# Optimization experiments

Hardware: AMD Instinct MI355X
Metric: run time of the kernel (lower is better)

The kernel has to match this reference:

```python
import jax, jax.numpy as jnp
import numpy as np

EMBED = 256
HEADS = 8
LAYERS = 6
FFN = 1024
LEVELS = 4
POINTS = 4
SHAPES = [(128, 128), (64, 64), (32, 32), (16, 16)]


def setup_inputs() -> dict:
    key = jax.random.key(0)
    ks = jax.random.split(key, 32)
    B = 2
    inp = {}
    for i, (h, w) in enumerate(SHAPES):
        inp[f'src{i}'] = jax.random.normal(ks[i], (B, EMBED, h, w), jnp.float32)
        inp[f'pos{i}'] = jax.random.normal(ks[4 + i], (B, EMBED, h, w), jnp.float32)
    s = 0.02
    inp['level_embed'] = jax.random.normal(ks[8], (LEVELS, EMBED), jnp.float32) * s
    inp['Wv'] = jax.random.normal(ks[9], (LAYERS, EMBED, EMBED), jnp.float32) * s
    inp['bv'] = jnp.zeros((LAYERS, EMBED), jnp.float32)
    inp['Woff'] = jax.random.normal(ks[10], (LAYERS, EMBED, HEADS * LEVELS * POINTS * 2), jnp.float32) * s
    inp['boff'] = jax.random.normal(ks[11], (LAYERS, HEADS * LEVELS * POINTS * 2), jnp.float32) * 0.5
    inp['Waw'] = jax.random.normal(ks[12], (LAYERS, EMBED, HEADS * LEVELS * POINTS), jnp.float32) * s
    inp['baw'] = jnp.zeros((LAYERS, HEADS * LEVELS * POINTS), jnp.float32)
    inp['Wout'] = jax.random.normal(ks[13], (LAYERS, EMBED, EMBED), jnp.float32) * s
    inp['bout'] = jnp.zeros((LAYERS, EMBED), jnp.float32)
    inp['gamma'] = jnp.ones((LAYERS, EMBED), jnp.float32)
    inp['beta'] = jnp.zeros((LAYERS, EMBED), jnp.float32)
    inp['W1'] = jax.random.normal(ks[14], (LAYERS, EMBED, FFN), jnp.float32) * s
    inp['b1'] = jnp.zeros((LAYERS, FFN), jnp.float32)
    inp['W2'] = jax.random.normal(ks[15], (LAYERS, FFN, EMBED), jnp.float32) * s
    inp['b2'] = jnp.zeros((LAYERS, EMBED), jnp.float32)
    return inp


def _layernorm(x, g, b, eps=1e-5):
    mu = x.mean(-1, keepdims=True)
    var = ((x - mu) ** 2).mean(-1, keepdims=True)
    return (x - mu) * jax.lax.rsqrt(var + eps) * g + b


def _bilinear_sample(value, loc, Hl, Wl):
    # value: [B, heads, S_l, Dh]; loc: [B, Len, heads, P, 2] normalized to [0,1]
    # grid_sample semantics: align_corners=False, zero padding
    B, Len, heads, P, _ = loc.shape
    Dh = value.shape[-1]
    x = loc[..., 0] * Wl - 0.5
    y = loc[..., 1] * Hl - 0.5
    x0 = jnp.floor(x)
    y0 = jnp.floor(y)
    dx = x - x0
    dy = y - y0
    x0i = x0.astype(jnp.int32)
    y0i = y0.astype(jnp.int32)
    out = jnp.zeros((B, heads, Len, P, Dh), value.dtype)
    corners = [(x0i, y0i, (1 - dx) * (1 - dy)), (x0i + 1, y0i, dx * (1 - dy)),
               (x0i, y0i + 1, (1 - dx) * dy), (x0i + 1, y0i + 1, dx * dy)]
    for xi, yi, w in corners:
        valid = (xi >= 0) & (xi < Wl) & (yi >= 0) & (yi < Hl)
        idx = jnp.clip(yi, 0, Hl - 1) * Wl + jnp.clip(xi, 0, Wl - 1)  # [B,Len,heads,P]
        idx_t = idx.transpose(0, 2, 1, 3).reshape(B, heads, Len * P)
        g = jnp.take_along_axis(value, idx_t[..., None], axis=2)  # [B,heads,Len*P,Dh]
        g = g.reshape(B, heads, Len, P, Dh)
        wv = jnp.where(valid, w, 0.0).transpose(0, 2, 1, 3)[..., None]  # [B,heads,Len,P,1]
        out = out + g * wv
    return out


def reference(src0, src1, src2, src3, pos0, pos1, pos2, pos3, level_embed,
              Wv, bv, Woff, boff, Waw, baw, Wout, bout, gamma, beta, W1, b1, W2, b2):
    srcs = [src0, src1, src2, src3]
    poss = [pos0, pos1, pos2, pos3]
    B, C = src0.shape[0], src0.shape[1]
    shapes = [(s.shape[2], s.shape[3]) for s in srcs]
    L = len(shapes)
    heads, P = HEADS, POINTS
    Dh = C // heads
    x = jnp.concatenate([s.reshape(B, C, -1).transpose(0, 2, 1) for s in srcs], axis=1)  # [B,Len,C]
    pos_flat = jnp.concatenate(
        [p.reshape(B, C, -1).transpose(0, 2, 1) + level_embed[l][None, None, :]
         for l, p in enumerate(poss)], axis=1)
    starts = np.concatenate([[0], np.cumsum([h * w for h, w in shapes])[:-1]]).tolist()
    # reference points (valid_ratios are all ones since masks are all-False)
    refs = []
    for (H, W) in shapes:
        yy, xx = jnp.meshgrid(jnp.linspace(0.5, H - 0.5, H), jnp.linspace(0.5, W - 0.5, W), indexing='ij')
        refs.append(jnp.stack([xx.reshape(-1) / W, yy.reshape(-1) / H], axis=-1))
    ref = jnp.concatenate(refs, axis=0)  # [Len,2]
    normalizer = jnp.array([[w, h] for h, w in shapes], dtype=x.dtype)  # [L,2]
    Len = x.shape[1]
    for li in range(LAYERS):
        q = x + pos_flat
        off = (q @ Woff[li] + boff[li]).reshape(B, Len, heads, L, P, 2)
        aw = jax.nn.softmax((q @ Waw[li] + baw[li]).reshape(B, Len, heads, L * P), axis=-1)
        aw = aw.reshape(B, Len, heads, L, P)
        loc = ref[None, :, None, None, None, :] + off / normalizer[None, None, None, :, None, :]
        v = (x @ Wv[li] + bv[li]).reshape(B, Len, heads, Dh).transpose(0, 2, 1, 3)  # [B,heads,Len,Dh]
        acc = jnp.zeros((B, heads, Len, Dh), x.dtype)
        for lvl, (H, W) in enumerate(shapes):
            s0 = starts[lvl]
            vl = v[:, :, s0:s0 + H * W, :]
            samp = _bilinear_sample(vl, loc[:, :, :, lvl], H, W)  # [B,heads,Len,P,Dh]
            awl = aw[:, :, :, lvl].transpose(0, 2, 1, 3)  # [B,heads,Len,P]
            acc = acc + (samp * awl[..., None]).sum(axis=3)
        attn_out = acc.transpose(0, 2, 1, 3).reshape(B, Len, C) @ Wout[li] + bout[li]
        x = x + attn_out  # dropout is identity at eval
        x = _layernorm(x, gamma[li], beta[li])
        x = jax.nn.relu(x @ W1[li] + b1[li]) @ W2[li] + b2[li]  # Mlp output (no residual, per source)
    return x
```

## Files before the change

kernel.cpp:

```cpp
#include <hip/hip_runtime.h>

#define LEN 21760
#define MROWS 43520
#define WSTRIDE 753664

typedef __attribute__((ext_vector_type(8))) short s8v;
typedef __attribute__((ext_vector_type(4))) short s4v;
typedef __attribute__((ext_vector_type(4))) float f4v;
typedef __attribute__((ext_vector_type(4))) unsigned u4v;

__device__ inline float bf2f(short u){
  union { unsigned u; float f; } v; v.u = ((unsigned)(unsigned short)u) << 16; return v.f;
}
__device__ inline short f2bf(float f){
  union { float f; unsigned u; } v; v.f = f;
  unsigned r = v.u + 0x7fffu + ((v.u >> 16) & 1u);
  return (short)(r >> 16);
}
__device__ inline void gload_lds16(const short* g, short* l){
  __builtin_amdgcn_global_load_lds((const __attribute__((address_space(1))) void*)g,
                                   (__attribute__((address_space(3))) void*)l, 16, 0, 0);
}

__global__ __launch_bounds__(256) void prep_kernel(
    const float* __restrict__ s0,const float* __restrict__ s1,
    const float* __restrict__ s2,const float* __restrict__ s3,
    const float* __restrict__ p0,const float* __restrict__ p1,
    const float* __restrict__ p2,const float* __restrict__ p3,
    const float* __restrict__ le,
    short* __restrict__ xbf, short* __restrict__ posb,
    short* __restrict__ q)
{
  __shared__ float xs[64][65];
  __shared__ float ps[64][65];
  const int n0 = blockIdx.x * 64;
  const int b  = blockIdx.y;
  const int t  = threadIdx.x;

  int l, s0n, lw;
  if (n0 < 16384){ l=0; s0n=0; lw=7; }
  else if (n0 < 20480){ l=1; s0n=16384; lw=6; }
  else if (n0 < 21504){ l=2; s0n=20480; lw=5; }
  else { l=3; s0n=21504; lw=4; }
  const int pbase = n0 - s0n;
  const long HW = 1L << (2*lw);
  const float* sp = (l==0?s0:(l==1?s1:(l==2?s2:s3)));
  const float* pp = (l==0?p0:(l==1?p1:(l==2?p2:p3)));

  for (int ch0 = 0; ch0 < 256; ch0 += 64){
    __syncthreads();
    #pragma unroll
    for (int cc = 0; cc < 4; cc++){
      int cl = cc*16 + (t >> 4);
      int quad = t & 15;
      int ch = ch0 + cl;
      long gi = (long)(b*256 + ch)*HW + pbase + quad*4;
      f4v xv = *(const f4v*)&sp[gi];
      f4v pv = *(const f4v*)&pp[gi];
      float lec = le[l*256 + ch];
      *(f4v*)&xs[cl][quad*4] = xv;
      f4v pe; pe[0]=pv[0]+lec; pe[1]=pv[1]+lec; pe[2]=pv[2]+lec; pe[3]=pv[3]+lec;
      *(f4v*)&ps[cl][quad*4] = pe;
    }
    __syncthreads();
    #pragma unroll
    for (int cc = 0; cc < 4; cc++){
      int pi = t >> 2;
      int cl = cc*16 + (t & 3)*4;
      long row = (long)b*LEN + n0 + pi;
      int col = ch0 + cl;
      s4v xv, pv, qv;
      #pragma unroll
      for (int j=0;j<4;j++){
        float xf = xs[cl+j][pi];
        float pf = ps[cl+j][pi];
        xv[j] = f2bf(xf); pv[j] = f2bf(pf);
        qv[j] = f2bf(xf + pf);
      }
      *(s4v*)&xbf[row*256 + col]  = xv;
      *(s4v*)&posb[row*256 + col] = pv;
      *(s4v*)&q[row*256 + col]    = qv;
    }
  }
}

__global__ void convw_kernel(const float* __restrict__ Woff, const float* __restrict__ Waw,
                             const float* __restrict__ Wv, const float* __restrict__ Wout,
                             const float* __restrict__ W1, const float* __restrict__ W2,
                             const float* __restrict__ boff, const float* __restrict__ baw,
                             short* __restrict__ wts, float* __restrict__ biasOA)
{
  int wid = blockIdx.y; int li = wid / 6; int w = wid % 6;
  const float* src; short* dst; int N, K;
  switch(w){
    case 0: src = Woff + li*65536;  dst = wts + (size_t)li*WSTRIDE;          N=256;  K=256;  break;
    case 1: src = Waw  + li*32768;  dst = wts + (size_t)li*WSTRIDE + 65536;  N=128;  K=256;  break;
    case 2: src = Wv   + li*65536;  dst = wts + (size_t)li*WSTRIDE + 98304;  N=256;  K=256;  break;
    case 3: src = Wout + li*65536;  dst = wts + (size_t)li*WSTRIDE + 163840; N=256;  K=256;  break;
    case 4: src = W1   + li*262144; dst = wts + (size_t)li*WSTRIDE + 229376; N=1024; K=256;  break;
    default:src = W2   + li*262144; dst = wts + (size_t)li*WSTRIDE + 491520; N=256;  K=1024; break;
  }
  int total = N*K;
  for (int i = blockIdx.x*blockDim.x + threadIdx.x; i < total; i += gridDim.x*blockDim.x){
    int n = i / K, k = i - n*K;
    dst[i] = f2bf(src[k*N + n]);
  }
  if (w == 1 && blockIdx.x == 0){
    for (int i = threadIdx.x; i < 384; i += blockDim.x){
      biasOA[li*384 + i] = (i < 256) ? boff[li*256 + i] : baw[li*128 + (i - 256)];
    }
  }
}

template<bool RELU, bool OUT_BF16, bool EMIT_Q>
__global__ __launch_bounds__(256) void gemm_bf16(
    const short* __restrict__ A, const short* __restrict__ Wt,
    const float* __restrict__ bias,
    void* __restrict__ Cout, const short* __restrict__ posb,
    short* __restrict__ qout,
    int M, int N, int K, int NT)
{
  __shared__ short As[128*64];
  __shared__ short Bs[128*64];
  const int p = blockIdx.x, nwg = gridDim.x;
  const int xq = nwg >> 3, xr = nwg & 7;
  const int xx = p & 7, xs2 = p >> 3;
  const int l = ((xx < xr) ? xx*(xq+1) : xr*(xq+1) + (xx-xr)*xq) + xs2;
  const int m0 = (l / NT) * 128;
  const int n0 = (l % NT) * 128;

  const int t = threadIdx.x;
  const int lane = t & 63, wv = t >> 6;
  const int wm = (wv >> 1) * 64, wn = (wv & 1) * 64;
  const int fr = lane & 15, fg = lane >> 4;
  const int srow = lane >> 3;
  const int schunk = (lane & 7) ^ (srow & 7);

  f4v acc[4][4];
  #pragma unroll
  for (int i=0;i<4;i++)
    #pragma unroll
    for (int j=0;j<4;j++) acc[i][j] = (f4v){0.f,0.f,0.f,0.f};

  for (int k0 = 0; k0 < K; k0 += 64) {
    __syncthreads();
    #pragma unroll
    for (int i=0;i<4;i++){
      int seg = wv*4 + i;
      int row = seg*8 + srow;
      gload_lds16(&A [(long)(m0+row)*K + k0 + schunk*8], &As[seg*512]);
      gload_lds16(&Wt[(long)(n0+row)*K + k0 + schunk*8], &Bs[seg*512]);
    }
    __syncthreads();
    #pragma unroll
    for (int kk=0; kk<64; kk+=32){
      s8v ar[4], br[4];
      #pragma unroll
      for (int i=0;i<4;i++){
        int r = wm + i*16 + fr;
        int ch = ((kk>>3) + fg) ^ (fr & 7);
        ar[i] = *(const s8v*)&As[r*64 + ch*8];
      }
      #pragma unroll
      for (int j=0;j<4;j++){
        int r = wn + j*16 + fr;
        int ch = ((kk>>3) + fg) ^ (fr & 7);
        br[j] = *(const s8v*)&Bs[r*64 + ch*8];
      }
      #pragma unroll
      for (int i=0;i<4;i++)
        #pragma unroll
        for (int j=0;j<4;j++)
          acc[i][j] = __builtin_amdgcn_mfma_f32_16x16x32_bf16(ar[i], br[j], acc[i][j], 0,0,0);
    }
  }
  #pragma unroll
  for (int i=0;i<4;i++){
    #pragma unroll
    for (int j=0;j<4;j++){
      int col = n0 + wn + j*16 + fr;
      float bcol = bias[col];
      #pragma unroll
      for (int r=0;r<4;r++){
        long row = m0 + wm + i*16 + fg*4 + r;
        float vv = acc[i][j][r] + bcol;
        if (RELU) vv = fmaxf(vv, 0.f);
        if (OUT_BF16) ((short*)Cout)[row*N + col] = f2bf(vv);
        else ((float*)Cout)[row*N + col] = vv;
        if (EMIT_Q){
          qout[row*N + col] = f2bf(vv + bf2f(posb[row*N + col]));
        }
      }
    }
  }
}

__global__ __launch_bounds__(512) void gemm_out_ln(
    const short* __restrict__ A, const short* __restrict__ Wt,
    const float* __restrict__ bias, const short* __restrict__ resid,
    const float* __restrict__ gamma, const float* __restrict__ beta,
    short* __restrict__ xln)
{
  const int K = 256;
  __shared__ short As[128*64];
  __shared__ short Bs[256*64];
  const int m0 = blockIdx.x * 128;
  const int t = threadIdx.x;
  const int lane = t & 63, wv = t >> 6;
  const int wm = wv * 16;
  const int fr = lane & 15, fg = lane >> 4;
  const int srow = lane >> 3;
  const int schunk = (lane & 7) ^ (srow & 7);

  f4v acc[16];
  #pragma unroll
  for (int j=0;j<16;j++) acc[j] = (f4v){0.f,0.f,0.f,0.f};

  for (int k0 = 0; k0 < K; k0 += 64) {
    __syncthreads();
    #pragma unroll
    for (int i=0;i<2;i++){
      int seg = wv*2 + i;
      int row = seg*8 + srow;
      gload_lds16(&A[(long)(m0+row)*K + k0 + schunk*8], &As[seg*512]);
    }
    #pragma unroll
    for (int i=0;i<4;i++){
      int seg = wv*4 + i;
      int row = seg*8 + srow;
      gload_lds16(&Wt[(long)row*K + k0 + schunk*8], &Bs[seg*512]);
    }
    __syncthreads();
    #pragma unroll
    for (int kk=0; kk<64; kk+=32){
      int ch = ((kk>>3) + fg);
      s8v ar = *(const s8v*)&As[(wm + fr)*64 + ((ch ^ (fr & 7)))*8];
      #pragma unroll
      for (int j=0;j<16;j++){
        s8v br = *(const s8v*)&Bs[(j*16 + fr)*64 + ((ch ^ (fr & 7)))*8];
        acc[j] = __builtin_amdgcn_mfma_f32_16x16x32_bf16(ar, br, acc[j], 0,0,0);
      }
    }
  }
  #pragma unroll
  for (int r=0;r<4;r++){
    long row = m0 + wm + fg*4 + r;
    float vals[16];
    float s = 0.f;
    #pragma unroll
    for (int j=0;j<16;j++){
      int col = j*16 + fr;
      float vv = acc[j][r] + bias[col] + bf2f(resid[row*256 + col]);
      vals[j] = vv; s += vv;
    }
    #pragma unroll
    for (int o=1;o<16;o<<=1) s += __shfl_xor(s, o, 64);
    float mu = s * (1.f/256.f);
    float s2 = 0.f;
    #pragma unroll
    for (int j=0;j<16;j++){ float d = vals[j]-mu; vals[j] = d; s2 += d*d; }
    #pragma unroll
    for (int o=1;o<16;o<<=1) s2 += __shfl_xor(s2, o, 64);
    float rstd = rsqrtf(s2*(1.f/256.f) + 1e-5f);
    #pragma unroll
    for (int j=0;j<16;j++){
      int col = j*16 + fr;
      xln[row*256 + col] = f2bf(vals[j]*rstd*gamma[col] + beta[col]);
    }
  }
}

__global__ __launch_bounds__(256) void sample_kernel(const short* __restrict__ v,
                const short* __restrict__ offaw, short* __restrict__ accO)
{
  const int t = threadIdx.x;
  const int qi = t >> 5;
  const int tq = t & 31;
  const int head = tq >> 2, cg = tq & 3;
  const int n = blockIdx.x * 8 + qi;
  const int b = blockIdx.y;
  const long m = (long)b*LEN + n;
  const short* oa = offaw + m*384;

  s8v or0 = *(const s8v*)&oa[head*32];
  s8v or1 = *(const s8v*)&oa[head*32 + 8];
  s8v or2 = *(const s8v*)&oa[head*32 + 16];
  s8v or3 = *(const s8v*)&oa[head*32 + 24];
  float off_f[32];
  #pragma unroll
  for (int i=0;i<8;i++){
    off_f[i]    = bf2f(or0[i]);
    off_f[8+i]  = bf2f(or1[i]);
    off_f[16+i] = bf2f(or2[i]);
    off_f[24+i] = bf2f(or3[i]);
  }

  s8v lg0 = *(const s8v*)&oa[256 + head*16];
  s8v lg1 = *(const s8v*)&oa[256 + head*16 + 8];
  float logit[16];
  #pragma unroll
  for (int i=0;i<8;i++){ logit[i] = bf2f(lg0[i]); logit[8+i] = bf2f(lg1[i]); }
  float mx = -1e30f;
  #pragma unroll
  for (int j=0;j<16;j++) mx = fmaxf(mx, logit[j]);
  float ssum = 0.f;
  #pragma unroll
  for (int j=0;j<16;j++){ logit[j] = __expf(logit[j]-mx); ssum += logit[j]; }
  float inv = 1.f/ssum;

  int s0n, lwn;
  if (n < 16384){ s0n=0; lwn=7; }
  else if (n < 20480){ s0n=16384; lwn=6; }
  else if (n < 21504){ s0n=20480; lwn=5; }
  else { s0n=21504; lwn=4; }
  int p = n - s0n;
  int Wn = 1 << lwn;
  float refx = ((p & (Wn-1)) + 0.5f) / Wn;
  float refy = ((p >> lwn) + 0.5f) / Wn;

  const int starts[4] = {0,16384,20480,21504};
  float acc[8];
  #pragma unroll
  for (int c=0;c<8;c++) acc[c] = 0.f;

  #pragma unroll
  for (int l=0;l<4;l++){
    const int W = 128 >> l, Wm1 = W - 1;
    const short* vb = v + ((long)b*LEN + starts[l])*256 + head*32 + cg*8;
    #pragma unroll
    for (int pp=0;pp<4;pp++){
      int j = l*4 + pp;
      float sx = refx * W + off_f[j*2]     - 0.5f;
      float sy = refy * W + off_f[j*2 + 1] - 0.5f;
      float fx0 = floorf(sx), fy0 = floorf(sy);
      float dx = sx - fx0, dy = sy - fy0;
      int x0 = (int)fx0, y0 = (int)fy0;
      int x0c = min(max(x0,0),Wm1),   x1c = min(max(x0+1,0),Wm1);
      int y0c = min(max(y0,0),Wm1),   y1c = min(max(y0+1,0),Wm1);
      float aw = logit[j] * inv;
      float r0w = ((unsigned)y0     < (unsigned)W) ? (1.f-dy)*aw : 0.f;
      float r1w = ((unsigned)(y0+1) < (unsigned)W) ? dy*aw       : 0.f;
      float c0w = ((unsigned)x0     < (unsigned)W) ? (1.f-dx)    : 0.f;
      float c1w = ((unsigned)(x0+1) < (unsigned)W) ? dx          : 0.f;
      float w00 = r0w*c0w, w10 = r0w*c1w, w01 = r1w*c0w, w11 = r1w*c1w;
      const short* r0p = vb + (long)(y0c*W)*256;
      const short* r1p = vb + (long)(y1c*W)*256;
      u4v g00 = *(const u4v*)&r0p[x0c*256];
      u4v g10 = *(const u4v*)&r0p[x1c*256];
      u4v g01 = *(const u4v*)&r1p[x0c*256];
      u4v g11 = *(const u4v*)&r1p[x1c*256];
      #pragma unroll
      for (int c=0;c<4;c++){
        union {unsigned u; float f;} lo00,hi00,lo10,hi10,lo01,hi01,lo11,hi11;
        lo00.u = g00[c] << 16;  hi00.u = g00[c];
        lo10.u = g10[c] << 16;  hi10.u = g10[c];
        lo01.u = g01[c] << 16;  hi01.u = g01[c];
        lo11.u = g11[c] << 16;  hi11.u = g11[c];
        acc[2*c]   += w00*lo00.f + w10*lo10.f + w01*lo01.f + w11*lo11.f;
        acc[2*c+1] += w00*hi00.f + w10*hi10.f + w01*hi01.f + w11*hi11.f;
      }
    }
  }
  s8v o;
  #pragma unroll
  for (int c=0;c<8;c++) o[c] = f2bf(acc[c]);
  *(s8v*)&accO[m*256 + head*32 + cg*8] = o;
}

extern "C" void kernel_launch(void* const* d_in, const int* in_sizes, int n_in,
                              void* d_out, int out_size, void* d_ws, size_t ws_size,
                              hipStream_t stream)
{
  const float* s0   = (const float*)d_in[0];
  const float* p0   = (const float*)d_in[1];
  const float* s1   = (const float*)d_in[2];
  const float* p1   = (const float*)d_in[3];
  const float* s2   = (const float*)d_in[4];
  const float* p2   = (const float*)d_in[5];
  const float* s3   = (const float*)d_in[6];
  const float* p3   = (const float*)d_in[7];
  const float* le   = (const float*)d_in[8];
  const float* Wv   = (const float*)d_in[9];
  const float* bv   = (const float*)d_in[10];
  const float* Woff = (const float*)d_in[11];
  const float* boff = (const float*)d_in[12];
  const float* Waw  = (const float*)d_in[13];
  const float* baw  = (const float*)d_in[14];
  const float* Wout = (const float*)d_in[15];
  const float* bout = (const float*)d_in[16];
  const float* gamma= (const float*)d_in[17];
  const float* beta = (const float*)d_in[18];
  const float* W1   = (const float*)d_in[19];
  const float* b1   = (const float*)d_in[20];
  const float* W2   = (const float*)d_in[21];
  const float* b2   = (const float*)d_in[22];

  char* wsb = (char*)d_ws;
  short* xbf   = (short*)(wsb);
  short* posb  = (short*)(wsb + 22282240);
  short* qxln  = (short*)(wsb + 44564480);
  short* vbf   = (short*)(wsb + 66846720);
  short* accb  = (short*)(wsb + 89128960);
  short* offawh= (short*)(wsb + 111411200);
  short* hbuf  = (short*)(wsb + 66846720);
  short* wts   = (short*)(wsb + 155975680);
  float* biasOA= (float*)(wsb + 165019648);

  prep_kernel<<<dim3(340,2),256,0,stream>>>(s0,s1,s2,s3,p0,p1,p2,p3,le,xbf,posb,qxln);
  convw_kernel<<<dim3(32,36),256,0,stream>>>(Woff,Waw,Wv,Wout,W1,W2,boff,baw,wts,biasOA);

  for (int li = 0; li < 6; li++){
    const short* wl = wts + (size_t)li*WSTRIDE;
    gemm_bf16<false,true,false><<<1020,256,0,stream>>>(
        qxln, wl, biasOA+li*384, offawh, nullptr,nullptr, MROWS, 384, 256, 3);
    gemm_bf16<false,true,false><<<680,256,0,stream>>>(
        xbf, wl+98304, bv+li*256, vbf, nullptr,nullptr, MROWS, 256, 256, 2);
    sample_kernel<<<dim3(LEN/8,2),256,0,stream>>>(vbf, offawh, accb);
    gemm_out_ln<<<340,512,0,stream>>>(accb, wl+163840, bout+li*256, xbf,
                                      gamma+li*256, beta+li*256, qxln);
    gemm_bf16<true,true,false><<<2720,256,0,stream>>>(
        qxln, wl+229376, b1+li*1024, hbuf, nullptr,nullptr, MROWS, 1024, 256, 8);
    if (li < 5){
      gemm_bf16<false,true,true><<<680,256,0,stream>>>(
          hbuf, wl+491520, b2+li*256, xbf, posb, qxln, MROWS, 256, 1024, 2);
    } else {
      gemm_bf16<false,false,false><<<680,256,0,stream>>>(
          hbuf, wl+491520, b2+li*256, (float*)d_out, nullptr,nullptr, MROWS, 256, 1024, 2);
    }
  }
}
```

Measured before the change: 1.445 ms.

## Precompute attention-weight softmax in separate kernel and remap sample block order

Moves the per-head softmax over the 16 attention logits out of the sampling kernel into a standalone kernel that overwrites the logits in place with bf16 probabilities. Each sample thread previously recomputed the softmax redundantly across its 4 channel groups. The sample kernel's block-to-query mapping is also permuted so that consecutive blocks spread across the level/spatial range, which may change cache locality and load balance. This adds an extra launch and a read/write pass over the logits, and the probabilities are now rounded to bf16.

```diff
diff --git a/kernel.cpp b/kernel.cpp
--- a/kernel.cpp
+++ b/kernel.cpp
@@ -270,6 +270,31 @@
   }
 }
 
+__global__ __launch_bounds__(256) void softmax_kernel(short* __restrict__ offaw)
+{
+  const int id = blockIdx.x*256 + threadIdx.x;
+  const long m = id >> 3;
+  const int h = id & 7;
+  short* oa = offaw + m*384 + 256 + h*16;
+  s8v lg0 = *(const s8v*)&oa[0];
+  s8v lg1 = *(const s8v*)&oa[8];
+  float lg[16];
+  #pragma unroll
+  for (int i=0;i<8;i++){ lg[i] = bf2f(lg0[i]); lg[8+i] = bf2f(lg1[i]); }
+  float mx = -1e30f;
+  #pragma unroll
+  for (int j=0;j<16;j++) mx = fmaxf(mx, lg[j]);
+  float ssum = 0.f;
+  #pragma unroll
+  for (int j=0;j<16;j++){ lg[j] = __expf(lg[j]-mx); ssum += lg[j]; }
+  float inv = 1.f/ssum;
+  s8v o0, o1;
+  #pragma unroll
+  for (int i=0;i<8;i++){ o0[i] = f2bf(lg[i]*inv); o1[i] = f2bf(lg[8+i]*inv); }
+  *(s8v*)&oa[0] = o0;
+  *(s8v*)&oa[8] = o1;
+}
+
 __global__ __launch_bounds__(256) void sample_kernel(const short* __restrict__ v,
                 const short* __restrict__ offaw, short* __restrict__ accO)
 {
@@ -277,7 +302,8 @@
   const int qi = t >> 5;
   const int tq = t & 31;
   const int head = tq >> 2, cg = tq & 3;
-  const int n = blockIdx.x * 8 + qi;
+  const int bid = blockIdx.x;
+  const int n = ((bid & 7) * 340 + (bid >> 3)) * 8 + qi;
   const int b = blockIdx.y;
   const long m = (long)b*LEN + n;
   const short* oa = offaw + m*384;
@@ -297,16 +323,9 @@
 
   s8v lg0 = *(const s8v*)&oa[256 + head*16];
   s8v lg1 = *(const s8v*)&oa[256 + head*16 + 8];
-  float logit[16];
-  #pragma unroll
-  for (int i=0;i<8;i++){ logit[i] = bf2f(lg0[i]); logit[8+i] = bf2f(lg1[i]); }
-  float mx = -1e30f;
-  #pragma unroll
-  for (int j=0;j<16;j++) mx = fmaxf(mx, logit[j]);
-  float ssum = 0.f;
-  #pragma unroll
-  for (int j=0;j<16;j++){ logit[j] = __expf(logit[j]-mx); ssum += logit[j]; }
-  float inv = 1.f/ssum;
+  float prob[16];
+  #pragma unroll
+  for (int i=0;i<8;i++){ prob[i] = bf2f(lg0[i]); prob[8+i] = bf2f(lg1[i]); }
 
   int s0n, lwn;
   if (n < 16384){ s0n=0; lwn=7; }
@@ -337,7 +356,7 @@
       int x0 = (int)fx0, y0 = (int)fy0;
       int x0c = min(max(x0,0),Wm1),   x1c = min(max(x0+1,0),Wm1);
       int y0c = min(max(y0,0),Wm1),   y1c = min(max(y0+1,0),Wm1);
-      float aw = logit[j] * inv;
+      float aw = prob[j];
       float r0w = ((unsigned)y0     < (unsigned)W) ? (1.f-dy)*aw : 0.f;
       float r1w = ((unsigned)(y0+1) < (unsigned)W) ? dy*aw       : 0.f;
       float c0w = ((unsigned)x0     < (unsigned)W) ? (1.f-dx)    : 0.f;
@@ -413,6 +432,7 @@
     const short* wl = wts + (size_t)li*WSTRIDE;
     gemm_bf16<false,true,false><<<1020,256,0,stream>>>(
         qxln, wl, biasOA+li*384, offawh, nullptr,nullptr, MROWS, 384, 256, 3);
+    softmax_kernel<<<1360,256,0,stream>>>(offawh);
     gemm_bf16<false,true,false><<<680,256,0,stream>>>(
         xbf, wl+98304, bv+li*256, vbf, nullptr,nullptr, MROWS, 256, 256, 2);
     sample_kernel<<<dim3(LEN/8,2),256,0,stream>>>(vbf, offawh, accb);
```

Result: no change. 1.457 ms (+0.8%).
